# Optimization experiments

Measured on AMD Instinct MI355X. Metric: run time of the kernel, lower is better.

Reference implementation:

```python
import jax, jax.numpy as jnp
import numpy as np

DIM = 4096
N_HEADS = 32
N_KV_HEADS = 8
HEAD_DIM = DIM // N_HEADS  # 128
N_REP = N_HEADS // N_KV_HEADS  # 4
BSZ_LIST = (16, 16)
START_POS_LIST = (2048, 1024)
SEQLEN = 1
CACHE_LEN = 2080
ROPE_THETA = 500000.0


def setup_inputs() -> dict:
    key = jax.random.key(0)
    ks = jax.random.split(key, 10)
    total_bsz = sum(BSZ_LIST)
    x = jax.random.normal(ks[0], (total_bsz, SEQLEN, DIM), dtype=jnp.float32)
    scale = 0.02
    wq = jax.random.normal(ks[1], (DIM, DIM), dtype=jnp.float32) * scale
    wk = jax.random.normal(ks[2], (N_KV_HEADS * HEAD_DIM, DIM), dtype=jnp.float32) * scale
    wv = jax.random.normal(ks[3], (N_KV_HEADS * HEAD_DIM, DIM), dtype=jnp.float32) * scale
    wo = jax.random.normal(ks[4], (DIM, DIM), dtype=jnp.float32) * scale
    cache_k0 = jax.random.normal(ks[5], (BSZ_LIST[0], CACHE_LEN, N_KV_HEADS, HEAD_DIM), dtype=jnp.float32)
    cache_v0 = jax.random.normal(ks[6], (BSZ_LIST[0], CACHE_LEN, N_KV_HEADS, HEAD_DIM), dtype=jnp.float32)
    cache_k1 = jax.random.normal(ks[7], (BSZ_LIST[1], CACHE_LEN, N_KV_HEADS, HEAD_DIM), dtype=jnp.float32)
    cache_v1 = jax.random.normal(ks[8], (BSZ_LIST[1], CACHE_LEN, N_KV_HEADS, HEAD_DIM), dtype=jnp.float32)
    # real RoPE tables (cos/sin of the complex freqs_cis)
    inv_freq = 1.0 / (ROPE_THETA ** (np.arange(0, HEAD_DIM, 2, dtype=np.float32) / HEAD_DIM))
    t = np.arange(CACHE_LEN, dtype=np.float32)
    ang = np.outer(t, inv_freq)  # [CACHE_LEN, HEAD_DIM/2]
    freqs_cos = jnp.asarray(np.cos(ang), dtype=jnp.float32)
    freqs_sin = jnp.asarray(np.sin(ang), dtype=jnp.float32)
    return {"x": x, "wq": wq, "wk": wk, "wv": wv, "wo": wo,
            "cache_k0": cache_k0, "cache_v0": cache_v0,
            "cache_k1": cache_k1, "cache_v1": cache_v1,
            "freqs_cos": freqs_cos, "freqs_sin": freqs_sin}


def _rope(v, cos, sin):
    # v: [b, s, h, d]; cos/sin: [s, d/2] -> interleaved complex rotation
    vr = v.reshape(v.shape[:-1] + (HEAD_DIM // 2, 2))
    a, b = vr[..., 0], vr[..., 1]
    c = cos[None, :, None, :]
    s = sin[None, :, None, :]
    out = jnp.stack([a * c - b * s, a * s + b * c], axis=-1)
    return out.reshape(v.shape)


def _group_attention(xq, xk, xv, cache_k, cache_v, start_pos, freqs_cos, freqs_sin):
    bsz, seqlen = xq.shape[0], xq.shape[1]
    cos = freqs_cos[start_pos:start_pos + seqlen]
    sin = freqs_sin[start_pos:start_pos + seqlen]
    xq = _rope(xq, cos, sin)
    xk = _rope(xk, cos, sin)
    # functional equivalent of cache[:, start_pos:start_pos+seqlen] = new; read [:start_pos+seqlen]
    keys = jnp.concatenate([cache_k[:, :start_pos], xk], axis=1)    # [b, kv, kvh, d]
    values = jnp.concatenate([cache_v[:, :start_pos], xv], axis=1)
    keys = jnp.repeat(keys, N_REP, axis=2)      # GQA repeat -> [b, kv, h, d]
    values = jnp.repeat(values, N_REP, axis=2)
    scores = jnp.einsum('bqhd,bkhd->bhqk', xq, keys) / jnp.sqrt(jnp.float32(HEAD_DIM))
    if seqlen > 1:
        kv_len = start_pos + seqlen
        q_pos = jnp.arange(seqlen)[:, None] + start_pos
        k_pos = jnp.arange(kv_len)[None, :]
        scores = jnp.where(k_pos <= q_pos, scores, jnp.float32(-jnp.inf))
    probs = jax.nn.softmax(scores.astype(jnp.float32), axis=-1).astype(xq.dtype)
    out = jnp.einsum('bhqk,bkhd->bqhd', probs, values)
    return out.reshape(bsz, seqlen, -1)


def reference(x, wq, wk, wv, wo, cache_k0, cache_v0, cache_k1, cache_v1, freqs_cos, freqs_sin):
    total_bsz, seqlen, _ = x.shape
    xq_ = x @ wq.T
    xk_ = x @ wk.T
    xv_ = x @ wv.T
    caches = ((cache_k0, cache_v0), (cache_k1, cache_v1))
    outputs = []
    start = 0
    for i, bsz in enumerate(BSZ_LIST):
        xq = xq_[start:start + bsz].reshape(bsz, seqlen, N_HEADS, HEAD_DIM)
        xk = xk_[start:start + bsz].reshape(bsz, seqlen, N_KV_HEADS, HEAD_DIM)
        xv = xv_[start:start + bsz].reshape(bsz, seqlen, N_KV_HEADS, HEAD_DIM)
        start += bsz
        ck, cv = caches[i]
        outputs.append(_group_attention(xq, xk, xv, ck, cv, START_POS_LIST[i], freqs_cos, freqs_sin))
    output = jnp.concatenate(outputs, axis=0)  # [total_bsz, seqlen, dim]
    return output @ wo.T
```

## Files before the change

kernel.cpp:

```cpp
#include <hip/hip_runtime.h>
#include <hip/hip_bf16.h>

#define DIM       4096
#define NHEADS    32
#define NKV       8
#define HD        128
#define NREP      4
#define CACHELEN  2080
#define QKVN      6144
#define BSZ       32
#define SP0       2048
#define SP1       1024
#define KCHUNK    512
#define NSPL      8
#define PSTRIDE   132

typedef unsigned short u16;
typedef unsigned int   u32;
typedef __bf16 bf16x8 __attribute__((ext_vector_type(8)));
typedef float  f32x4  __attribute__((ext_vector_type(4)));

static __device__ __forceinline__ bf16x8 pack8(float4 lo, float4 hi) {
    bf16x8 r;
    r[0] = (__bf16)lo.x; r[1] = (__bf16)lo.y; r[2] = (__bf16)lo.z; r[3] = (__bf16)lo.w;
    r[4] = (__bf16)hi.x; r[5] = (__bf16)hi.y; r[6] = (__bf16)hi.z; r[7] = (__bf16)hi.w;
    return r;
}

__global__ __launch_bounds__(256) void qkv_gemm(
    const float* __restrict__ x, const float* __restrict__ wq,
    const float* __restrict__ wk, const float* __restrict__ wv,
    float* __restrict__ qkv_acc)
{
    const int lane = threadIdx.x & 63;
    const int w    = threadIdx.x >> 6;
    const int n0   = (blockIdx.x * 4 + w) * 16;
    const float* W; int nr;
    if (n0 < 4096)      { W = wq; nr = n0; }
    else if (n0 < 5120) { W = wk; nr = n0 - 4096; }
    else                { W = wv; nr = n0 - 5120; }
    const int c16  = lane & 15;
    const int quad = lane >> 4;
    const int k0   = blockIdx.y * KCHUNK;
    const float* ap0 = x + (size_t)c16 * DIM + k0 + quad * 8;
    const float* ap1 = ap0 + 16 * DIM;
    const float* bp  = W + (size_t)(nr + c16) * DIM + k0 + quad * 8;
    f32x4 acc0 = {0.f,0.f,0.f,0.f}, acc1 = {0.f,0.f,0.f,0.f};
#pragma unroll 4
    for (int kk = 0; kk < KCHUNK; kk += 32) {
        bf16x8 a0 = pack8(*(const float4*)(ap0 + kk), *(const float4*)(ap0 + kk + 4));
        bf16x8 a1 = pack8(*(const float4*)(ap1 + kk), *(const float4*)(ap1 + kk + 4));
        bf16x8 b  = pack8(*(const float4*)(bp  + kk), *(const float4*)(bp  + kk + 4));
        acc0 = __builtin_amdgcn_mfma_f32_16x16x32_bf16(a0, b, acc0, 0, 0, 0);
        acc1 = __builtin_amdgcn_mfma_f32_16x16x32_bf16(a1, b, acc1, 0, 0, 0);
    }
#pragma unroll
    for (int r = 0; r < 4; ++r) {
        int m = quad * 4 + r;
        atomicAdd(&qkv_acc[(size_t)m * QKVN + n0 + c16], acc0[r]);
        atomicAdd(&qkv_acc[(size_t)(m + 16) * QKVN + n0 + c16], acc1[r]);
    }
}

__global__ __launch_bounds__(256) void attn_decode_split(
    const float* __restrict__ qkv,
    const float* __restrict__ ck0, const float* __restrict__ cv0,
    const float* __restrict__ ck1, const float* __restrict__ cv1,
    const float* __restrict__ fcos, const float* __restrict__ fsin,
    float* __restrict__ part)
{
    const int tid  = threadIdx.x;
    const int lane = tid & 63;
    const int w    = tid >> 6;
    const int quad = lane >> 4;
    const int ch   = lane & 15;
    const int db   = ch * 8;

    const int s = blockIdx.x & (NSPL - 1);
    const int g = (blockIdx.x >> 3) & 7;
    const int b = blockIdx.x >> 6;

    int sp; const float *CK, *CV;
    if (b < 16) { sp = SP0; size_t off = (size_t)b * CACHELEN * NKV * HD; CK = ck0 + off; CV = cv0 + off; }
    else        { sp = SP1; size_t off = (size_t)(b - 16) * CACHELEN * NKV * HD; CK = ck1 + off; CV = cv1 + off; }

    const int rps = sp / NSPL;

    float cs[4], sn[4];
#pragma unroll
    for (int i = 0; i < 4; ++i) {
        int fi = sp * (HD / 2) + ch * 4 + i;
        cs[i] = fcos[fi];
        sn[i] = fsin[fi];
    }
    const float rs = 0.08838834764831845f;

    float qv[4][8];
#pragma unroll
    for (int h = 0; h < 4; ++h) {
        const float* qp = qkv + (size_t)b * QKVN + (g * 4 + h) * HD + db;
        float t[8];
#pragma unroll
        for (int j = 0; j < 8; ++j) t[j] = qp[j];
#pragma unroll
        for (int i = 0; i < 4; ++i) {
            float e = t[2 * i], o = t[2 * i + 1];
            qv[h][2 * i]     = (e * cs[i] - o * sn[i]) * rs;
            qv[h][2 * i + 1] = (e * sn[i] + o * cs[i]) * rs;
        }
    }

    float m_[4] = {-INFINITY, -INFINITY, -INFINITY, -INFINITY};
    float l_[4] = {0.f, 0.f, 0.f, 0.f};
    float acc[4][8];
#pragma unroll
    for (int h = 0; h < 4; ++h)
#pragma unroll
        for (int j = 0; j < 8; ++j) acc[h][j] = 0.f;

    const size_t rstride = NKV * HD;
    const float* kbase = CK + g * HD + db;
    const float* vbase = CV + g * HD + db;

    auto process = [&](const float* kf, const float* vf) {
        float d0 = 0.f, d1 = 0.f, d2 = 0.f, d3 = 0.f;
#pragma unroll
        for (int j = 0; j < 8; ++j) {
            d0 = fmaf(qv[0][j], kf[j], d0);
            d1 = fmaf(qv[1][j], kf[j], d1);
            d2 = fmaf(qv[2][j], kf[j], d2);
            d3 = fmaf(qv[3][j], kf[j], d3);
        }
#pragma unroll
        for (int off = 1; off < 16; off <<= 1) {
            d0 += __shfl_xor(d0, off);
            d1 += __shfl_xor(d1, off);
            d2 += __shfl_xor(d2, off);
            d3 += __shfl_xor(d3, off);
        }
        float sc[4] = {d0, d1, d2, d3};
#pragma unroll
        for (int h = 0; h < 4; ++h) {
            float mn = fmaxf(m_[h], sc[h]);
            float sl = __expf(m_[h] - mn);
            float p  = __expf(sc[h] - mn);
            l_[h] = l_[h] * sl + p;
#pragma unroll
            for (int j = 0; j < 8; ++j)
                acc[h][j] = fmaf(acc[h][j], sl, p * vf[j]);
            m_[h] = mn;
        }
    };

    const int iters = rps >> 5;
    const int base  = s * rps;
    for (int it = 0; it < iters; ++it) {
        int r0 = base + it * 32 + w * 8 + quad;
        const float* kp0 = kbase + (size_t)r0 * rstride;
        const float* vp0 = vbase + (size_t)r0 * rstride;
        float K0[8], V0[8], K1[8], V1[8];
        *(float4*)(K0)     = *(const float4*)kp0;
        *(float4*)(K0 + 4) = *(const float4*)(kp0 + 4);
        *(float4*)(V0)     = *(const float4*)vp0;
        *(float4*)(V0 + 4) = *(const float4*)(vp0 + 4);
        *(float4*)(K1)     = *(const float4*)(kp0 + 4 * rstride);
        *(float4*)(K1 + 4) = *(const float4*)(kp0 + 4 * rstride + 4);
        *(float4*)(V1)     = *(const float4*)(vp0 + 4 * rstride);
        *(float4*)(V1 + 4) = *(const float4*)(vp0 + 4 * rstride + 4);
        process(K0, V0);
        process(K1, V1);
    }

    if (s == 0) {
        float kn[8], vn[8];
        const float* kp = qkv + (size_t)b * QKVN + 4096 + g * HD + db;
        const float* vp = qkv + (size_t)b * QKVN + 5120 + g * HD + db;
        float t[8];
#pragma unroll
        for (int j = 0; j < 8; ++j) t[j] = kp[j];
#pragma unroll
        for (int i = 0; i < 4; ++i) {
            float e = t[2 * i], o = t[2 * i + 1];
            kn[2 * i]     = e * cs[i] - o * sn[i];
            kn[2 * i + 1] = e * sn[i] + o * cs[i];
        }
#pragma unroll
        for (int j = 0; j < 8; ++j) vn[j] = vp[j];

        float d0 = 0.f, d1 = 0.f, d2 = 0.f, d3 = 0.f;
#pragma unroll
        for (int j = 0; j < 8; ++j) {
            d0 = fmaf(qv[0][j], kn[j], d0);
            d1 = fmaf(qv[1][j], kn[j], d1);
            d2 = fmaf(qv[2][j], kn[j], d2);
            d3 = fmaf(qv[3][j], kn[j], d3);
        }
#pragma unroll
        for (int off = 1; off < 16; off <<= 1) {
            d0 += __shfl_xor(d0, off);
            d1 += __shfl_xor(d1, off);
            d2 += __shfl_xor(d2, off);
            d3 += __shfl_xor(d3, off);
        }
        if (w == 0 && quad == 0) {
            float sc[4] = {d0, d1, d2, d3};
#pragma unroll
            for (int h = 0; h < 4; ++h) {
                float mn = fmaxf(m_[h], sc[h]);
                float sl = __expf(m_[h] - mn);
                float p  = __expf(sc[h] - mn);
                l_[h] = l_[h] * sl + p;
#pragma unroll
                for (int j = 0; j < 8; ++j)
                    acc[h][j] = fmaf(acc[h][j], sl, p * vn[j]);
                m_[h] = mn;
            }
        }
    }

#pragma unroll
    for (int off = 16; off <= 32; off <<= 1) {
#pragma unroll
        for (int h = 0; h < 4; ++h) {
            float mo = __shfl_xor(m_[h], off);
            float lo = __shfl_xor(l_[h], off);
            float ao[8];
#pragma unroll
            for (int j = 0; j < 8; ++j) ao[j] = __shfl_xor(acc[h][j], off);
            float mn = fmaxf(m_[h], mo);
            float s1 = __expf(m_[h] - mn);
            float s2 = __expf(mo - mn);
            l_[h] = l_[h] * s1 + lo * s2;
#pragma unroll
            for (int j = 0; j < 8; ++j) acc[h][j] = acc[h][j] * s1 + ao[j] * s2;
            m_[h] = mn;
        }
    }

    __shared__ float ls_m[4][4][16];
    __shared__ float ls_l[4][4][16];
    __shared__ float ls_a[4][4][16][8];
    if (quad == 0) {
#pragma unroll
        for (int h = 0; h < 4; ++h) {
            ls_m[w][h][ch] = m_[h];
            ls_l[w][h][ch] = l_[h];
#pragma unroll
            for (int j = 0; j < 8; ++j) ls_a[w][h][ch][j] = acc[h][j];
        }
    }
    __syncthreads();
    if (tid < 64) {
        int h = tid >> 4, c = tid & 15;
        float mm = -INFINITY, ll = 0.f, ac[8] = {0.f,0.f,0.f,0.f,0.f,0.f,0.f,0.f};
#pragma unroll
        for (int w2 = 0; w2 < 4; ++w2) {
            float m2 = ls_m[w2][h][c], l2 = ls_l[w2][h][c];
            float mn = fmaxf(mm, m2);
            float s1 = __expf(mm - mn), s2 = __expf(m2 - mn);
            ll = ll * s1 + l2 * s2;
#pragma unroll
            for (int j = 0; j < 8; ++j) ac[j] = ac[j] * s1 + ls_a[w2][h][c][j] * s2;
            mm = mn;
        }
        float* pp = part + ((((size_t)(b * 8 + g) * NSPL + s) * 4 + h) * PSTRIDE);
        float4 o0, o1;
        o0.x = ac[0]; o0.y = ac[1]; o0.z = ac[2]; o0.w = ac[3];
        o1.x = ac[4]; o1.y = ac[5]; o1.z = ac[6]; o1.w = ac[7];
        *(float4*)(pp + c * 8)     = o0;
        *(float4*)(pp + c * 8 + 4) = o1;
        if (c == 0) { pp[128] = mm; pp[129] = ll; }
    }
}

__global__ __launch_bounds__(64) void attn_reduce(
    const float* __restrict__ part, float* __restrict__ attn)
{
    const int lane = threadIdx.x;
    const int h = lane >> 4, c = lane & 15;
    const int bg = blockIdx.x;
    const float* pb = part + (size_t)bg * NSPL * 4 * PSTRIDE;

    float mm = -INFINITY, ll = 0.f, ac[8] = {0.f,0.f,0.f,0.f,0.f,0.f,0.f,0.f};
#pragma unroll
    for (int s = 0; s < NSPL; ++s) {
        const float* pp = pb + ((size_t)s * 4 + h) * PSTRIDE;
        float m2 = pp[128], l2 = pp[129];
        float4 a0 = *(const float4*)(pp + c * 8);
        float4 a1 = *(const float4*)(pp + c * 8 + 4);
        float a2[8] = {a0.x, a0.y, a0.z, a0.w, a1.x, a1.y, a1.z, a1.w};
        float mn = fmaxf(mm, m2);
        float s1 = __expf(mm - mn), s2 = __expf(m2 - mn);
        ll = ll * s1 + l2 * s2;
#pragma unroll
        for (int j = 0; j < 8; ++j) ac[j] = ac[j] * s1 + a2[j] * s2;
        mm = mn;
    }
    float inv = 1.f / ll;
    const int b = bg >> 3, g = bg & 7;
    float* op = attn + (size_t)b * DIM + (g * 4 + h) * HD + c * 8;
    float4 o0, o1;
    o0.x = ac[0] * inv; o0.y = ac[1] * inv; o0.z = ac[2] * inv; o0.w = ac[3] * inv;
    o1.x = ac[4] * inv; o1.y = ac[5] * inv; o1.z = ac[6] * inv; o1.w = ac[7] * inv;
    *(float4*)op       = o0;
    *(float4*)(op + 4) = o1;
}

__global__ __launch_bounds__(256) void out_gemm(
    const float* __restrict__ A, const float* __restrict__ wo,
    float* __restrict__ out)
{
    const int lane = threadIdx.x & 63;
    const int w    = threadIdx.x >> 6;
    const int n0   = (blockIdx.x * 4 + w) * 16;
    const int c16  = lane & 15;
    const int quad = lane >> 4;
    const int k0   = blockIdx.y * KCHUNK;
    const float* ap0 = A + (size_t)c16 * DIM + k0 + quad * 8;
    const float* ap1 = ap0 + 16 * DIM;
    const float* bp  = wo + (size_t)(n0 + c16) * DIM + k0 + quad * 8;
    f32x4 acc0 = {0.f,0.f,0.f,0.f}, acc1 = {0.f,0.f,0.f,0.f};
#pragma unroll 4
    for (int kk = 0; kk < KCHUNK; kk += 32) {
        bf16x8 a0 = pack8(*(const float4*)(ap0 + kk), *(const float4*)(ap0 + kk + 4));
        bf16x8 a1 = pack8(*(const float4*)(ap1 + kk), *(const float4*)(ap1 + kk + 4));
        bf16x8 b  = pack8(*(const float4*)(bp  + kk), *(const float4*)(bp  + kk + 4));
        acc0 = __builtin_amdgcn_mfma_f32_16x16x32_bf16(a0, b, acc0, 0, 0, 0);
        acc1 = __builtin_amdgcn_mfma_f32_16x16x32_bf16(a1, b, acc1, 0, 0, 0);
    }
#pragma unroll
    for (int r = 0; r < 4; ++r) {
        int m = quad * 4 + r;
        atomicAdd(&out[(size_t)m * DIM + n0 + c16], acc0[r]);
        atomicAdd(&out[(size_t)(m + 16) * DIM + n0 + c16], acc1[r]);
    }
}

extern "C" void kernel_launch(void* const* d_in, const int* in_sizes, int n_in,
                              void* d_out, int out_size, void* d_ws, size_t ws_size,
                              hipStream_t stream)
{
    const float* x   = (const float*)d_in[0];
    const float* wq  = (const float*)d_in[1];
    const float* wk  = (const float*)d_in[2];
    const float* wv  = (const float*)d_in[3];
    const float* wo  = (const float*)d_in[4];
    const float* ck0 = (const float*)d_in[5];
    const float* cv0 = (const float*)d_in[6];
    const float* ck1 = (const float*)d_in[7];
    const float* cv1 = (const float*)d_in[8];
    const float* fc  = (const float*)d_in[9];
    const float* fs  = (const float*)d_in[10];

    float* qkv_acc = (float*)d_ws;
    float* attn    = qkv_acc + BSZ * QKVN;
    float* part    = attn + BSZ * DIM;
    float* out     = (float*)d_out;

    hipMemsetAsync(qkv_acc, 0, (size_t)(BSZ * QKVN) * sizeof(float), stream);
    hipMemsetAsync(out, 0, (size_t)(BSZ * DIM) * sizeof(float), stream);

    qkv_gemm<<<dim3(QKVN / 64, DIM / KCHUNK), 256, 0, stream>>>(x, wq, wk, wv, qkv_acc);
    attn_decode_split<<<dim3(BSZ * NKV * NSPL), 256, 0, stream>>>(qkv_acc, ck0, cv0, ck1, cv1, fc, fs, part);
    attn_reduce<<<dim3(BSZ * NKV), 64, 0, stream>>>(part, attn);
    out_gemm<<<dim3(DIM / 64, DIM / KCHUNK), 256, 0, stream>>>(attn, wo, out);
}
```

Measured before the change: 573.4 us.

## Balance attention splits by fixed row chunks, prefetch KV, shrink GEMM K-chunk

The attention kernel now gives each block a fixed 128-row chunk, so the longer-context group gets 16 splits and the shorter gets 8, instead of both using 8 splits of unequal length. This is meant to balance work across blocks and raise parallelism. The inner loop is fully unrolled and software-pipelined, loading the next K/V rows while the current pair is processed, and two rows share one online-softmax update. KCHUNK is halved, which doubles the GEMM split-K grid at the cost of more atomics. The partial buffer is sized for 16 splits, and the reduce kernel loops over a variable split count.

```diff
diff --git a/kernel.cpp b/kernel.cpp
--- a/kernel.cpp
+++ b/kernel.cpp
@@ -11,14 +11,19 @@
 #define BSZ       32
 #define SP0       2048
 #define SP1       1024
-#define KCHUNK    512
-#define NSPL      8
+#define KCHUNK    256
+#define SPLITROWS 128
+#define MAXSPL    16
 #define PSTRIDE   132
 
 typedef unsigned short u16;
 typedef unsigned int   u32;
 typedef __bf16 bf16x8 __attribute__((ext_vector_type(8)));
 typedef float  f32x4  __attribute__((ext_vector_type(4)));
+
+#define LD8(dst, p) do { \
+    *(float4*)(dst)       = *(const float4*)(p); \
+    *(float4*)((dst) + 4) = *(const float4*)((p) + 4); } while (0)
 
 static __device__ __forceinline__ bf16x8 pack8(float4 lo, float4 hi) {
     bf16x8 r;
@@ -76,15 +81,19 @@
     const int ch   = lane & 15;
     const int db   = ch * 8;
 
-    const int s = blockIdx.x & (NSPL - 1);
-    const int g = (blockIdx.x >> 3) & 7;
-    const int b = blockIdx.x >> 6;
-
-    int sp; const float *CK, *CV;
-    if (b < 16) { sp = SP0; size_t off = (size_t)b * CACHELEN * NKV * HD; CK = ck0 + off; CV = cv0 + off; }
-    else        { sp = SP1; size_t off = (size_t)(b - 16) * CACHELEN * NKV * HD; CK = ck1 + off; CV = cv1 + off; }
-
-    const int rps = sp / NSPL;
+    int b, g, s, sp;
+    const float *CK, *CV;
+    if ((int)blockIdx.x < 2048) {
+        int bid = blockIdx.x;
+        b = bid >> 7; g = (bid >> 4) & 7; s = bid & 15; sp = SP0;
+        size_t off = (size_t)b * CACHELEN * NKV * HD;
+        CK = ck0 + off; CV = cv0 + off;
+    } else {
+        int bid = blockIdx.x - 2048;
+        b = 16 + (bid >> 6); g = (bid >> 3) & 7; s = bid & 7; sp = SP1;
+        size_t off = (size_t)(b - 16) * CACHELEN * NKV * HD;
+        CK = ck1 + off; CV = cv1 + off;
+    }
 
     float cs[4], sn[4];
 #pragma unroll
@@ -122,14 +131,92 @@
     const float* kbase = CK + g * HD + db;
     const float* vbase = CV + g * HD + db;
 
-    auto process = [&](const float* kf, const float* vf) {
+    auto process2 = [&](const float* k0, const float* v0,
+                        const float* k1, const float* v1) {
+        float d[8];
+#pragma unroll
+        for (int i = 0; i < 8; ++i) d[i] = 0.f;
+#pragma unroll
+        for (int j = 0; j < 8; ++j) {
+#pragma unroll
+            for (int h = 0; h < 4; ++h) {
+                d[h]     = fmaf(qv[h][j], k0[j], d[h]);
+                d[4 + h] = fmaf(qv[h][j], k1[j], d[4 + h]);
+            }
+        }
+#pragma unroll
+        for (int off = 1; off < 16; off <<= 1) {
+#pragma unroll
+            for (int i = 0; i < 8; ++i) d[i] += __shfl_xor(d[i], off);
+        }
+#pragma unroll
+        for (int h = 0; h < 4; ++h) {
+            float mn = fmaxf(fmaxf(m_[h], d[h]), d[4 + h]);
+            float sl = __expf(m_[h] - mn);
+            float p0 = __expf(d[h] - mn);
+            float p1 = __expf(d[4 + h] - mn);
+            l_[h] = l_[h] * sl + p0 + p1;
+#pragma unroll
+            for (int j = 0; j < 8; ++j)
+                acc[h][j] = fmaf(p1, v1[j], fmaf(p0, v0[j], acc[h][j] * sl));
+            m_[h] = mn;
+        }
+    };
+
+    {
+        const int r0 = s * SPLITROWS + w * 8 + quad;
+        const float* kp = kbase + (size_t)r0 * rstride;
+        const float* vp = vbase + (size_t)r0 * rstride;
+        float K0[8], V0[8], K1[8], V1[8];
+        float nK0[8], nV0[8], nK1[8], nV1[8];
+        LD8(K0, kp);
+        LD8(K1, kp + 4 * rstride);
+        LD8(V0, vp);
+        LD8(V1, vp + 4 * rstride);
+#pragma unroll
+        for (int it = 0; it < 4; ++it) {
+            if (it < 3) {
+                const float* kq = kp + (size_t)(it + 1) * 32 * rstride;
+                const float* vq = vp + (size_t)(it + 1) * 32 * rstride;
+                LD8(nK0, kq);
+                LD8(nK1, kq + 4 * rstride);
+                LD8(nV0, vq);
+                LD8(nV1, vq + 4 * rstride);
+            }
+            process2(K0, V0, K1, V1);
+            if (it < 3) {
+#pragma unroll
+                for (int j = 0; j < 8; ++j) {
+                    K0[j] = nK0[j]; K1[j] = nK1[j];
+                    V0[j] = nV0[j]; V1[j] = nV1[j];
+                }
+            }
+        }
+    }
+
+    if (s == 0) {
+        float kn[8], vn[8];
+        const float* kp = qkv + (size_t)b * QKVN + 4096 + g * HD + db;
+        const float* vp = qkv + (size_t)b * QKVN + 5120 + g * HD + db;
+        float t[8];
+#pragma unroll
+        for (int j = 0; j < 8; ++j) t[j] = kp[j];
+#pragma unroll
+        for (int i = 0; i < 4; ++i) {
+            float e = t[2 * i], o = t[2 * i + 1];
+            kn[2 * i]     = e * cs[i] - o * sn[i];
+            kn[2 * i + 1] = e * sn[i] + o * cs[i];
+        }
+#pragma unroll
+        for (int j = 0; j < 8; ++j) vn[j] = vp[j];
+
         float d0 = 0.f, d1 = 0.f, d2 = 0.f, d3 = 0.f;
 #pragma unroll
         for (int j = 0; j < 8; ++j) {
-            d0 = fmaf(qv[0][j], kf[j], d0);
-            d1 = fmaf(qv[1][j], kf[j], d1);
-            d2 = fmaf(qv[2][j], kf[j], d2);
-            d3 = fmaf(qv[3][j], kf[j], d3);
+            d0 = fmaf(qv[0][j], kn[j], d0);
+            d1 = fmaf(qv[1][j], kn[j], d1);
+            d2 = fmaf(qv[2][j], kn[j], d2);
+            d3 = fmaf(qv[3][j], kn[j], d3);
         }
 #pragma unroll
         for (int off = 1; off < 16; off <<= 1) {
@@ -138,70 +225,6 @@
             d2 += __shfl_xor(d2, off);
             d3 += __shfl_xor(d3, off);
         }
-        float sc[4] = {d0, d1, d2, d3};
-#pragma unroll
-        for (int h = 0; h < 4; ++h) {
-            float mn = fmaxf(m_[h], sc[h]);
-            float sl = __expf(m_[h] - mn);
-            float p  = __expf(sc[h] - mn);
-            l_[h] = l_[h] * sl + p;
-#pragma unroll
-            for (int j = 0; j < 8; ++j)
-                acc[h][j] = fmaf(acc[h][j], sl, p * vf[j]);
-            m_[h] = mn;
-        }
-    };
-
-    const int iters = rps >> 5;
-    const int base  = s * rps;
-    for (int it = 0; it < iters; ++it) {
-        int r0 = base + it * 32 + w * 8 + quad;
-        const float* kp0 = kbase + (size_t)r0 * rstride;
-        const float* vp0 = vbase + (size_t)r0 * rstride;
-        float K0[8], V0[8], K1[8], V1[8];
-        *(float4*)(K0)     = *(const float4*)kp0;
-        *(float4*)(K0 + 4) = *(const float4*)(kp0 + 4);
-        *(float4*)(V0)     = *(const float4*)vp0;
-        *(float4*)(V0 + 4) = *(const float4*)(vp0 + 4);
-        *(float4*)(K1)     = *(const float4*)(kp0 + 4 * rstride);
-        *(float4*)(K1 + 4) = *(const float4*)(kp0 + 4 * rstride + 4);
-        *(float4*)(V1)     = *(const float4*)(vp0 + 4 * rstride);
-        *(float4*)(V1 + 4) = *(const float4*)(vp0 + 4 * rstride + 4);
-        process(K0, V0);
-        process(K1, V1);
-    }
-
-    if (s == 0) {
-        float kn[8], vn[8];
-        const float* kp = qkv + (size_t)b * QKVN + 4096 + g * HD + db;
-        const float* vp = qkv + (size_t)b * QKVN + 5120 + g * HD + db;
-        float t[8];
-#pragma unroll
-        for (int j = 0; j < 8; ++j) t[j] = kp[j];
-#pragma unroll
-        for (int i = 0; i < 4; ++i) {
-            float e = t[2 * i], o = t[2 * i + 1];
-            kn[2 * i]     = e * cs[i] - o * sn[i];
-            kn[2 * i + 1] = e * sn[i] + o * cs[i];
-        }
-#pragma unroll
-        for (int j = 0; j < 8; ++j) vn[j] = vp[j];
-
-        float d0 = 0.f, d1 = 0.f, d2 = 0.f, d3 = 0.f;
-#pragma unroll
-        for (int j = 0; j < 8; ++j) {
-            d0 = fmaf(qv[0][j], kn[j], d0);
-            d1 = fmaf(qv[1][j], kn[j], d1);
-            d2 = fmaf(qv[2][j], kn[j], d2);
-            d3 = fmaf(qv[3][j], kn[j], d3);
-        }
-#pragma unroll
-        for (int off = 1; off < 16; off <<= 1) {
-            d0 += __shfl_xor(d0, off);
-            d1 += __shfl_xor(d1, off);
-            d2 += __shfl_xor(d2, off);
-            d3 += __shfl_xor(d3, off);
-        }
         if (w == 0 && quad == 0) {
             float sc[4] = {d0, d1, d2, d3};
 #pragma unroll
@@ -263,7 +286,8 @@
             for (int j = 0; j < 8; ++j) ac[j] = ac[j] * s1 + ls_a[w2][h][c][j] * s2;
             mm = mn;
         }
-        float* pp = part + ((((size_t)(b * 8 + g) * NSPL + s) * 4 + h) * PSTRIDE);
+        int bg = b * 8 + g;
+        float* pp = part + ((((size_t)bg * MAXSPL + s) * 4 + h) * PSTRIDE);
         float4 o0, o1;
         o0.x = ac[0]; o0.y = ac[1]; o0.z = ac[2]; o0.w = ac[3];
         o1.x = ac[4]; o1.y = ac[5]; o1.z = ac[6]; o1.w = ac[7];
@@ -279,11 +303,12 @@
     const int lane = threadIdx.x;
     const int h = lane >> 4, c = lane & 15;
     const int bg = blockIdx.x;
-    const float* pb = part + (size_t)bg * NSPL * 4 * PSTRIDE;
+    const int b = bg >> 3, g = bg & 7;
+    const int nspl = (b < 16) ? (SP0 / SPLITROWS) : (SP1 / SPLITROWS);
+    const float* pb = part + (size_t)bg * MAXSPL * 4 * PSTRIDE;
 
     float mm = -INFINITY, ll = 0.f, ac[8] = {0.f,0.f,0.f,0.f,0.f,0.f,0.f,0.f};
-#pragma unroll
-    for (int s = 0; s < NSPL; ++s) {
+    for (int s = 0; s < nspl; ++s) {
         const float* pp = pb + ((size_t)s * 4 + h) * PSTRIDE;
         float m2 = pp[128], l2 = pp[129];
         float4 a0 = *(const float4*)(pp + c * 8);
@@ -297,7 +322,6 @@
         mm = mn;
     }
     float inv = 1.f / ll;
-    const int b = bg >> 3, g = bg & 7;
     float* op = attn + (size_t)b * DIM + (g * 4 + h) * HD + c * 8;
     float4 o0, o1;
     o0.x = ac[0] * inv; o0.y = ac[1] * inv; o0.z = ac[2] * inv; o0.w = ac[3] * inv;
@@ -361,7 +385,7 @@
     hipMemsetAsync(out, 0, (size_t)(BSZ * DIM) * sizeof(float), stream);
 
     qkv_gemm<<<dim3(QKVN / 64, DIM / KCHUNK), 256, 0, stream>>>(x, wq, wk, wv, qkv_acc);
-    attn_decode_split<<<dim3(BSZ * NKV * NSPL), 256, 0, stream>>>(qkv_acc, ck0, cv0, ck1, cv1, fc, fs, part);
+    attn_decode_split<<<dim3(2048 + 1024), 256, 0, stream>>>(qkv_acc, ck0, cv0, ck1, cv1, fc, fs, part);
     attn_reduce<<<dim3(BSZ * NKV), 64, 0, stream>>>(part, attn);
     out_gemm<<<dim3(DIM / 64, DIM / KCHUNK), 256, 0, stream>>>(attn, wo, out);
 }
```

Result: slower. 589.7 us (+2.8%).
